# Performance work log

Hardware: AMD Instinct MI355X
Metric: run time of the kernel (lower is better)

The kernel has to match this reference:

```python
import jax, jax.numpy as jnp
import numpy as np
from jax import lax

SOS_TOKEN = 0
PAD_LEN = 30  # tokenizer.pad_len -> number of greedy decode steps


def _gru_cell(x, h, w_ih, w_hh, b_ih, b_hh):
    # PyTorch GRU cell math. x,h: [B,H]; w_*: [3H,H]; b_*: [3H]
    gi = x @ w_ih.T + b_ih
    gh = h @ w_hh.T + b_hh
    i_r, i_z, i_n = jnp.split(gi, 3, axis=-1)
    h_r, h_z, h_n = jnp.split(gh, 3, axis=-1)
    r = jax.nn.sigmoid(i_r + h_r)
    z = jax.nn.sigmoid(i_z + h_z)
    n = jnp.tanh(i_n + r * h_n)
    return (1.0 - z) * n + z * h


def _sm_encode(sm_hidden, conv_w, conv_b, enc_w, enc_b):
    # sm_hidden: [B, L, C] -> conv over time with C input channels
    x = jnp.transpose(sm_hidden, (0, 2, 1))  # [B, C, L]
    conv = lax.conv_general_dilated(
        x, conv_w, window_strides=(1,), padding='VALID',
        dimension_numbers=('NCH', 'OIH', 'NCH'))  # [B, O, L-k+1]
    conv = jax.nn.relu(conv + conv_b[None, :, None])
    pooled = jnp.max(conv, axis=-1)  # [B, O]
    return jax.nn.relu(pooled @ enc_w.T + enc_b)  # [B, H]


def reference(sm_hidden, embedding, w_ih, w_hh, b_ih, b_hh,
              w_out, b_out, conv_w, conv_b, enc_w, enc_b):
    B = sm_hidden.shape[0]
    h0 = _sm_encode(sm_hidden, conv_w, conv_b, enc_w, enc_b)  # [B, H]

    # The original re-runs the GRU over the whole (append-only) prefix each
    # iteration; since the GRU is deterministic this equals incremental
    # single-step updates, which we do here.
    def step(carry, _):
        h, tok = carry
        emb = embedding[tok]                      # [B, H]
        h_new = _gru_cell(emb, h, w_ih, w_hh, b_ih, b_hh)
        logits = h_new @ w_out.T + b_out          # [B, V]
        tok_new = jnp.argmax(logits, axis=-1)     # greedy topk(1)
        return (h_new, tok_new), (h_new, tok_new)

    tok0 = jnp.full((B,), SOS_TOKEN, dtype=jnp.int32)
    (h_last, _), (hiddens, toks) = lax.scan(step, (h0, tok0), None, length=PAD_LEN)

    decoder_output = jax.nn.log_softmax(h_last @ w_out.T + b_out, axis=1)  # [B, V]
    decoder_hidden = hiddens  # [PAD_LEN, B, H] == rnn_out of final _base_forward
    decoded_indices = jnp.concatenate([tok0[None, :], toks], axis=0)  # [PAD_LEN+1, B]
    return decoder_output, decoder_hidden, decoded_indices


def setup_inputs() -> dict:
    key = jax.random.key(0)
    ks = jax.random.split(key, 12)
    B, L, C = 512, 120, 128
    H, V, O, K = 1024, 512, 32, 10
    s = 1.0 / np.sqrt(H)
    return {
        'sm_hidden': jax.random.normal(ks[0], (B, L, C), jnp.float32),
        'embedding': jax.random.normal(ks[1], (V, H), jnp.float32),
        'w_ih': jax.random.uniform(ks[2], (3 * H, H), jnp.float32, -s, s),
        'w_hh': jax.random.uniform(ks[3], (3 * H, H), jnp.float32, -s, s),
        'b_ih': jax.random.uniform(ks[4], (3 * H,), jnp.float32, -s, s),
        'b_hh': jax.random.uniform(ks[5], (3 * H,), jnp.float32, -s, s),
        'w_out': jax.random.uniform(ks[6], (V, H), jnp.float32, -s, s),
        'b_out': jax.random.uniform(ks[7], (V,), jnp.float32, -s, s),
        'conv_w': jax.random.normal(ks[8], (O, C, K), jnp.float32) * 0.05,
        'conv_b': jax.random.normal(ks[9], (O,), jnp.float32) * 0.05,
        'enc_w': jax.random.uniform(ks[10], (H, O), jnp.float32, -s, s),
        'enc_b': jax.random.uniform(ks[11], (H,), jnp.float32, -s, s),
    }
```

## Files before the change

kernel.cpp:

```cpp
#include <hip/hip_runtime.h>
#include <hip/hip_bf16.h>
#include <math.h>

#define Bsz 512
#define Hd 1024
#define Vd 512
#define Cc 128
#define Ll 120
#define Kk 10
#define Oo 32
#define NSTEP 30

typedef __attribute__((ext_vector_type(8))) short bf16x8;
typedef __attribute__((ext_vector_type(4))) float f32x4;
typedef unsigned short ushort;
typedef unsigned long long u64;

static __device__ __forceinline__ float sigm(float x) { return 1.f / (1.f + expf(-x)); }
static __device__ __forceinline__ ushort f2bf(float x) {
    __hip_bfloat16 h = __float2bfloat16(x);
    return *(ushort*)&h;
}
static __device__ __forceinline__ float bf2f(ushort u) {
    __hip_bfloat16 h; *(ushort*)&h = u;
    return __bfloat162float(h);
}
static __device__ __forceinline__ unsigned monofy(float f) {
    unsigned u = __float_as_uint(f);
    return (u & 0x80000000u) ? ~u : (u | 0x80000000u);
}

__global__ void k_pack(const float* __restrict__ W, ushort* __restrict__ hi,
                       ushort* __restrict__ lo, int total) {
    int idx = blockIdx.x * 256 + threadIdx.x;
    if (idx >= total) return;
    int jj = idx & 7, l = (idx >> 3) & 63, c = (idx >> 9) & 31, nf = idx >> 14;
    int n = nf * 16 + (l & 15);
    int k = c * 32 + ((l >> 4) << 3) + jj;
    float v = W[(size_t)n * 1024 + k];
    ushort h = f2bf(v);
    hi[idx] = h;
    lo[idx] = f2bf(v - bf2f(h));
}

__global__ void k_packconv(const float* __restrict__ cw, ushort* __restrict__ hi,
                           ushort* __restrict__ lo) {
    int idx = blockIdx.x * 256 + threadIdx.x;
    if (idx >= 2 * 40 * 64 * 8) return;
    int jj = idx & 7, l = (idx >> 3) & 63, ch = (idx >> 9) % 40, nf = idx / (40 * 512);
    int o = nf * 16 + (l & 15);
    int k = ch * 32 + ((l >> 4) << 3) + jj;
    int kc = k >> 7, c = k & 127;
    float v = cw[(o * Cc + c) * Kk + kc];
    ushort h = f2bf(v);
    hi[idx] = h;
    lo[idx] = f2bf(v - bf2f(h));
}

__global__ __launch_bounds__(256) void k_convmfma(const float* __restrict__ sm,
                                                  const ushort* __restrict__ wH,
                                                  const ushort* __restrict__ wL,
                                                  const float* __restrict__ cb,
                                                  const float* __restrict__ ew,
                                                  const float* __restrict__ eb,
                                                  float* __restrict__ h0,
                                                  ushort* __restrict__ ApHi,
                                                  ushort* __restrict__ ApLo) {
    __shared__ ushort hiS[137 * 128];
    __shared__ ushort loS[137 * 128];
    __shared__ float sred[4][2][16];
    __shared__ float ps[Oo];
    int b = blockIdx.x, tid = threadIdx.x, wid = tid >> 6, l = tid & 63;

    const float* smb = sm + (size_t)b * (Ll * Cc);
    for (int i = tid; i < 1920; i += 256) {
        int row = i >> 4, col0 = (i & 15) * 8;
        float4 fa = *(const float4*)(smb + row * Cc + col0);
        float4 fb = *(const float4*)(smb + row * Cc + col0 + 4);
        float vv[8] = {fa.x, fa.y, fa.z, fa.w, fb.x, fb.y, fb.z, fb.w};
        ushort h8[8], l8[8];
#pragma unroll
        for (int q = 0; q < 8; ++q) {
            ushort h = f2bf(vv[q]);
            h8[q] = h;
            l8[q] = f2bf(vv[q] - bf2f(h));
        }
        int o = ((row << 8) + (col0 << 1)) ^ ((row & 7) << 4);
        *(bf16x8*)((char*)hiS + o) = *(bf16x8*)h8;
        *(bf16x8*)((char*)loS + o) = *(bf16x8*)l8;
    }
    __syncthreads();

    f32x4 acc[2][2];
#pragma unroll
    for (int i = 0; i < 2; ++i)
#pragma unroll
        for (int j = 0; j < 2; ++j) acc[i][j] = (f32x4)0.f;

    bf16x8 aH0[2], aL0[2], bH0[2], bL0[2];
    bf16x8 aH1[2], aL1[2], bH1[2], bL1[2];

#define CLD(AH, AL, BH, BL, ch)                                                        \
    {                                                                                  \
        _Pragma("unroll") for (int tf2 = 0; tf2 < 2; ++tf2) {                          \
            int row = (wid * 2 + tf2) * 16 + (l & 15) + ((ch) >> 2);                   \
            int o = ((row << 8) + ((((ch) & 3) * 32 + ((l >> 4) << 3)) << 1))          \
                    ^ ((row & 7) << 4);                                                \
            AH[tf2] = *(const bf16x8*)((const char*)hiS + o);                          \
            AL[tf2] = *(const bf16x8*)((const char*)loS + o);                          \
        }                                                                              \
        _Pragma("unroll") for (int nf = 0; nf < 2; ++nf) {                             \
            int boff = ((nf * 40 + (ch)) * 64 + l) * 8;                                \
            BH[nf] = *(const bf16x8*)(wH + boff);                                      \
            BL[nf] = *(const bf16x8*)(wL + boff);                                      \
        }                                                                              \
    }
#define CST(AH, AL, BH, BL)                                                            \
    {                                                                                  \
        _Pragma("unroll") for (int tf2 = 0; tf2 < 2; ++tf2)                            \
            _Pragma("unroll") for (int nf = 0; nf < 2; ++nf) {                         \
                acc[tf2][nf] = __builtin_amdgcn_mfma_f32_16x16x32_bf16(                \
                    AH[tf2], BH[nf], acc[tf2][nf], 0, 0, 0);                           \
                acc[tf2][nf] = __builtin_amdgcn_mfma_f32_16x16x32_bf16(                \
                    AH[tf2], BL[nf], acc[tf2][nf], 0, 0, 0);                           \
                acc[tf2][nf] = __builtin_amdgcn_mfma_f32_16x16x32_bf16(                \
                    AL[tf2], BH[nf], acc[tf2][nf], 0, 0, 0);                           \
            }                                                                          \
    }

    CLD(aH0, aL0, bH0, bL0, 0)
#pragma unroll
    for (int ch = 0; ch < 40; ch += 2) {
        CLD(aH1, aL1, bH1, bL1, ch + 1)
        CST(aH0, aL0, bH0, bL0)
        if (ch + 2 < 40) CLD(aH0, aL0, bH0, bL0, ch + 2)
        CST(aH1, aL1, bH1, bL1)
    }
#undef CLD
#undef CST

    float mx[2] = {-1e38f, -1e38f};
#pragma unroll
    for (int tf2 = 0; tf2 < 2; ++tf2) {
        int tb = (wid * 2 + tf2) * 16 + ((l >> 4) << 2);
#pragma unroll
        for (int q = 0; q < 4; ++q) {
            if (tb + q <= 110) {
                mx[0] = fmaxf(mx[0], acc[tf2][0][q]);
                mx[1] = fmaxf(mx[1], acc[tf2][1][q]);
            }
        }
    }
#pragma unroll
    for (int s = 16; s < 64; s <<= 1) {
        mx[0] = fmaxf(mx[0], __shfl_xor(mx[0], s));
        mx[1] = fmaxf(mx[1], __shfl_xor(mx[1], s));
    }
    if (l < 16) {
        sred[wid][0][l] = mx[0];
        sred[wid][1][l] = mx[1];
    }
    __syncthreads();
    if (tid < Oo) {
        float m = sred[0][tid >> 4][tid & 15];
#pragma unroll
        for (int w = 1; w < 4; ++w) m = fmaxf(m, sred[w][tid >> 4][tid & 15]);
        ps[tid] = fmaxf(m + cb[tid], 0.f);
    }
    __syncthreads();
    for (int j = tid; j < Hd; j += 256) {
        float a = eb[j];
        const float4* e4 = (const float4*)(ew + (size_t)j * Oo);
#pragma unroll
        for (int c4 = 0; c4 < 8; ++c4) {
            float4 w = e4[c4];
            a += ps[c4 * 4 + 0] * w.x + ps[c4 * 4 + 1] * w.y +
                 ps[c4 * 4 + 2] * w.z + ps[c4 * 4 + 3] * w.w;
        }
        a = fmaxf(a, 0.f);
        h0[(size_t)b * Hd + j] = a;
        ushort hb = f2bf(a);
        ushort lb = f2bf(a - bf2f(hb));
        int c = j >> 5, sub = (j >> 3) & 3, jj = j & 7, amf = b >> 4;
        int lane_r = (b & 15) + (sub << 4);
        int flat = ((amf * 32 + c) * 64 + lane_r) * 8 + jj;
        ApHi[flat] = hb;
        ApLo[flat] = lb;
    }
}

template <int EPI>
__global__ __launch_bounds__(512, 2) void k_rnn(const ushort* __restrict__ Ah,
                                                const ushort* __restrict__ Al,
                                                const ushort* __restrict__ Bh,
                                                const ushort* __restrict__ Bl,
                                                const float* __restrict__ bias,
                                                float* __restrict__ outF,
                                                const float* __restrict__ gi_all,
                                                const u64* __restrict__ pkRd,
                                                u64* __restrict__ pkWr,
                                                float* __restrict__ outIdxRow,
                                                const float* __restrict__ hOld,
                                                ushort* __restrict__ ApHi,
                                                ushort* __restrict__ ApLo) {
    __shared__ ushort Bs[2][48][512];
    int id = blockIdx.x;
    int xcd = id & 7, r = id >> 3;
    int jt = xcd * 4 + (r & 3);
    int mt = r >> 2;
    int tid = threadIdx.x, wid = tid >> 6, l = tid & 63;
    int wm = wid >> 1, wj = wid & 1;
    int mf = mt * 4 + wm;
    int jf = jt * 2 + wj;
    int jcol = jf * 16 + (l & 15);

    float giR[4][3], hR[4];
    int bR[4], tkR[4];
    if constexpr (EPI == 1) {
#pragma unroll
        for (int q = 0; q < 4; ++q) {
            bR[q] = mf * 16 + ((l >> 4) << 2) + q;
            u64 pk = pkRd[bR[q]];
            tkR[q] = 511 - (int)(unsigned)(pk & 0xFFFFFFFFu);
            const float* gi = gi_all + (size_t)tkR[q] * 3072;
            giR[q][0] = gi[jcol];
            giR[q][1] = gi[1024 + jcol];
            giR[q][2] = gi[2048 + jcol];
            hR[q] = hOld[(size_t)bR[q] * 1024 + jcol];
        }
        if (jt == 0 && wj == 0 && (l & 15) == 0) {
#pragma unroll
            for (int q = 0; q < 4; ++q) {
                pkWr[bR[q]] = 0ULL;
                if (outIdxRow) outIdxRow[bR[q]] = (float)tkR[q];
            }
        }
    }

    f32x4 acc[3];
#pragma unroll
    for (int g = 0; g < 3; ++g) acc[g] = (f32x4)0.f;

    bf16x8 stg[6], aH0[4], aL0[4], aH1[4], aL1[4];

#define STG_LD(it)                                                                     \
    {                                                                                  \
        _Pragma("unroll") for (int k = 0; k < 6; ++k) {                                \
            int u = wid + 8 * k;                                                       \
            int hl = u & 1, wjb = (u >> 1) & 1, g = (u >> 2) % 3, cu = u / 12;         \
            const ushort* sp = hl ? Bl : Bh;                                           \
            stg[k] = *(const bf16x8*)(sp +                                             \
                (size_t)(((g * 64 + jt * 2 + wjb) * 32 + (it) * 4 + cu) * 64 + l) * 8);\
        }                                                                              \
    }
#define STG_WR(buf)                                                                    \
    {                                                                                  \
        _Pragma("unroll") for (int k = 0; k < 6; ++k)                                  \
            *(bf16x8*)&Bs[buf][wid + 8 * k][l * 8] = stg[k];                           \
    }
#define A_LD(DH, DL, it)                                                               \
    {                                                                                  \
        _Pragma("unroll") for (int cc = 0; cc < 4; ++cc) {                             \
            DH[cc] = *(const bf16x8*)(Ah + (size_t)((mf * 32 + (it) * 4 + cc) * 64 + l) * 8); \
            DL[cc] = *(const bf16x8*)(Al + (size_t)((mf * 32 + (it) * 4 + cc) * 64 + l) * 8); \
        }                                                                              \
    }
#define CMP(buf, AH, AL)                                                               \
    {                                                                                  \
        _Pragma("unroll") for (int cc = 0; cc < 4; ++cc)                               \
            _Pragma("unroll") for (int g = 0; g < 3; ++g) {                            \
                bf16x8 bhh = *(const bf16x8*)&Bs[buf][cc * 12 + g * 4 + wj * 2 + 0][l * 8]; \
                bf16x8 bll = *(const bf16x8*)&Bs[buf][cc * 12 + g * 4 + wj * 2 + 1][l * 8]; \
                acc[g] = __builtin_amdgcn_mfma_f32_16x16x32_bf16(AH[cc], bhh, acc[g], 0, 0, 0); \
                acc[g] = __builtin_amdgcn_mfma_f32_16x16x32_bf16(AH[cc], bll, acc[g], 0, 0, 0); \
                acc[g] = __builtin_amdgcn_mfma_f32_16x16x32_bf16(AL[cc], bhh, acc[g], 0, 0, 0); \
            }                                                                          \
    }

    STG_LD(0)
    STG_WR(0)
    STG_LD(1)
    A_LD(aH0, aL0, 0)
    __syncthreads();
#pragma unroll
    for (int it = 0; it < 8; ++it) {
        int buf = it & 1;
        if (it < 7) STG_WR(buf ^ 1)
        if (it < 6) STG_LD(it + 2)
        if (it & 1) {
            if (it < 7) A_LD(aH0, aL0, it + 1)
            CMP(buf, aH1, aL1)
        } else {
            if (it < 7) A_LD(aH1, aL1, it + 1)
            CMP(buf, aH0, aL0)
        }
        __syncthreads();
    }
#undef STG_LD
#undef STG_WR
#undef A_LD
#undef CMP

    if constexpr (EPI == 0) {
#pragma unroll
        for (int q = 0; q < 4; ++q) {
            int b = mf * 16 + ((l >> 4) << 2) + q;
#pragma unroll
            for (int g = 0; g < 3; ++g)
                outF[(size_t)b * 3072 + g * 1024 + jcol] =
                    acc[g][q] + bias[g * 1024 + jcol];
        }
    } else {
        float bj0 = bias[jcol], bj1 = bias[1024 + jcol], bj2 = bias[2048 + jcol];
        int c = jcol >> 5, sub = (jcol >> 3) & 3, jj = jcol & 7;
#pragma unroll
        for (int q = 0; q < 4; ++q) {
            int b = bR[q];
            float rr = sigm(giR[q][0] + acc[0][q] + bj0);
            float zz = sigm(giR[q][1] + acc[1][q] + bj1);
            float nn = tanhf(giR[q][2] + rr * (acc[2][q] + bj2));
            float hv = (1.f - zz) * nn + zz * hR[q];
            outF[(size_t)b * 1024 + jcol] = hv;
            ushort hb = f2bf(hv);
            ushort lb = f2bf(hv - bf2f(hb));
            int lane_r = (b & 15) + (sub << 4);
            int flat = (((b >> 4) * 32 + c) * 64 + lane_r) * 8 + jj;
            ApHi[flat] = hb;
            ApLo[flat] = lb;
        }
    }
}

__global__ __launch_bounds__(256) void k_lgt(const ushort* __restrict__ Ah,
                                             const ushort* __restrict__ Al,
                                             const ushort* __restrict__ Bh,
                                             const ushort* __restrict__ Bl,
                                             const float* __restrict__ bias,
                                             float* __restrict__ outF,
                                             u64* __restrict__ pkOut) {
    int p = blockIdx.x * 4 + (threadIdx.x >> 6);
    int l = threadIdx.x & 63;
    int mf = p >> 5, vf = p & 31;
    size_t ab = (size_t)(mf * 32) * 512 + l * 8;
    size_t bb = (size_t)(vf * 32) * 512 + l * 8;
    f32x4 acc = (f32x4)0.f;
    bf16x8 a0h, a0l, b0h, b0l, a1h, a1l, b1h, b1l;

#define LD1(AH, AL, BH, BL, c)                                                         \
    {                                                                                  \
        AH = *(const bf16x8*)(Ah + ab + (size_t)(c) * 512);                            \
        AL = *(const bf16x8*)(Al + ab + (size_t)(c) * 512);                            \
        BH = *(const bf16x8*)(Bh + bb + (size_t)(c) * 512);                            \
        BL = *(const bf16x8*)(Bl + bb + (size_t)(c) * 512);                            \
    }
#define ST1(AH, AL, BH, BL)                                                            \
    {                                                                                  \
        acc = __builtin_amdgcn_mfma_f32_16x16x32_bf16(AH, BH, acc, 0, 0, 0);           \
        acc = __builtin_amdgcn_mfma_f32_16x16x32_bf16(AH, BL, acc, 0, 0, 0);           \
        acc = __builtin_amdgcn_mfma_f32_16x16x32_bf16(AL, BH, acc, 0, 0, 0);           \
    }

    LD1(a0h, a0l, b0h, b0l, 0)
#pragma unroll
    for (int c = 0; c < 32; c += 2) {
        LD1(a1h, a1l, b1h, b1l, c + 1)
        ST1(a0h, a0l, b0h, b0l)
        if (c + 2 < 32) LD1(a0h, a0l, b0h, b0l, c + 2)
        ST1(a1h, a1l, b1h, b1l)
    }
#undef LD1
#undef ST1

    int v = vf * 16 + (l & 15);
    float bv = bias[v];
    float lg[4];
    unsigned vmq[4];
#pragma unroll
    for (int q = 0; q < 4; ++q) {
        int b = mf * 16 + ((l >> 4) << 2) + q;
        lg[q] = acc[q] + bv;
        outF[(size_t)b * Vd + v] = lg[q];
        vmq[q] = 511u - (unsigned)v;
    }
#pragma unroll
    for (int off = 1; off < 16; off <<= 1) {
#pragma unroll
        for (int q = 0; q < 4; ++q) {
            float og = __shfl_xor(lg[q], off);
            unsigned ov = __shfl_xor(vmq[q], off);
            if (og > lg[q] || (og == lg[q] && ov > vmq[q])) { lg[q] = og; vmq[q] = ov; }
        }
    }
    if ((l & 15) == 0) {
#pragma unroll
        for (int q = 0; q < 4; ++q) {
            int b = mf * 16 + ((l >> 4) << 2) + q;
            u64 pk = ((u64)monofy(lg[q]) << 32) | (u64)vmq[q];
            atomicMax(&pkOut[b], pk);
        }
    }
}

__global__ __launch_bounds__(64) void k_fin(const float* __restrict__ logits,
                                            const u64* __restrict__ pk,
                                            float* __restrict__ out_lsm,
                                            float* __restrict__ outIdxRow) {
    int b = blockIdx.x, l = threadIdx.x;
    const float* row = logits + (size_t)b * Vd;
    float bv = -3.4e38f;
#pragma unroll
    for (int s = 0; s < 8; ++s) bv = fmaxf(bv, row[s * 64 + l]);
#pragma unroll
    for (int off = 1; off < 64; off <<= 1) bv = fmaxf(bv, __shfl_xor(bv, off));
    float sum = 0.f;
#pragma unroll
    for (int s = 0; s < 8; ++s) sum += expf(row[s * 64 + l] - bv);
#pragma unroll
    for (int off = 1; off < 64; off <<= 1) sum += __shfl_xor(sum, off);
    float lse = logf(sum) + bv;
#pragma unroll
    for (int s = 0; s < 8; ++s) {
        int v = s * 64 + l;
        out_lsm[(size_t)b * Vd + v] = row[v] - lse;
    }
    if (l == 0)
        outIdxRow[b] = (float)(511 - (int)(unsigned)(pk[b] & 0xFFFFFFFFu));
}

__global__ void k_init(u64* __restrict__ P0, float* __restrict__ out_idx0) {
    int i = blockIdx.x * 64 + threadIdx.x;
    if (i < Bsz) {
        P0[i] = (1ULL << 32) | 511ULL;
        out_idx0[i] = 0.f;
    }
}

extern "C" void kernel_launch(void* const* d_in, const int* in_sizes, int n_in,
                              void* d_out, int out_size, void* d_ws, size_t ws_size,
                              hipStream_t stream) {
    const float* sm    = (const float*)d_in[0];
    const float* emb   = (const float*)d_in[1];
    const float* w_ih  = (const float*)d_in[2];
    const float* w_hh  = (const float*)d_in[3];
    const float* b_ih  = (const float*)d_in[4];
    const float* b_hh  = (const float*)d_in[5];
    const float* w_out = (const float*)d_in[6];
    const float* b_out = (const float*)d_in[7];
    const float* cw    = (const float*)d_in[8];
    const float* cb    = (const float*)d_in[9];
    const float* ew    = (const float*)d_in[10];
    const float* eb    = (const float*)d_in[11];

    float* out0 = (float*)d_out;
    float* out1 = out0 + (size_t)Bsz * Vd;
    float* out2 = out1 + (size_t)NSTEP * Bsz * Hd;

    char* wsp = (char*)d_ws;
    float*  f_gi  = (float*)wsp;  wsp += sizeof(float) * Bsz * 3072;
    float*  f_h0  = (float*)wsp;  wsp += sizeof(float) * Bsz * Hd;
    float*  f_log = (float*)wsp;  wsp += sizeof(float) * Bsz * Vd;
    u64*    Ppk0  = (u64*)wsp;    wsp += sizeof(u64) * Bsz;
    u64*    Ppk1  = (u64*)wsp;    wsp += sizeof(u64) * Bsz;
    ushort* ApHi0 = (ushort*)wsp; wsp += sizeof(ushort) * Bsz * Hd;
    ushort* ApLo0 = (ushort*)wsp; wsp += sizeof(ushort) * Bsz * Hd;
    ushort* ApHi1 = (ushort*)wsp; wsp += sizeof(ushort) * Bsz * Hd;
    ushort* ApLo1 = (ushort*)wsp; wsp += sizeof(ushort) * Bsz * Hd;
    ushort* embH  = (ushort*)wsp; wsp += sizeof(ushort) * Vd * Hd;
    ushort* embL  = (ushort*)wsp; wsp += sizeof(ushort) * Vd * Hd;
    ushort* wihH  = (ushort*)wsp; wsp += sizeof(ushort) * 3072 * Hd;
    ushort* wihL  = (ushort*)wsp; wsp += sizeof(ushort) * 3072 * Hd;
    ushort* whhH  = (ushort*)wsp; wsp += sizeof(ushort) * 3072 * Hd;
    ushort* whhL  = (ushort*)wsp; wsp += sizeof(ushort) * 3072 * Hd;
    ushort* woutH = (ushort*)wsp; wsp += sizeof(ushort) * Vd * Hd;
    ushort* woutL = (ushort*)wsp; wsp += sizeof(ushort) * Vd * Hd;
    ushort* cwBH  = (ushort*)wsp; wsp += sizeof(ushort) * 2 * 40 * 64 * 8;
    ushort* cwBL  = (ushort*)wsp; wsp += sizeof(ushort) * 2 * 40 * 64 * 8;

    k_packconv<<<160, 256, 0, stream>>>(cw, cwBH, cwBL);
    k_pack<<<(3072 * 1024) / 256, 256, 0, stream>>>(w_ih, wihH, wihL, 3072 * 1024);
    k_pack<<<(3072 * 1024) / 256, 256, 0, stream>>>(w_hh, whhH, whhL, 3072 * 1024);
    k_pack<<<(512 * 1024) / 256, 256, 0, stream>>>(w_out, woutH, woutL, 512 * 1024);
    k_pack<<<(512 * 1024) / 256, 256, 0, stream>>>(emb, embH, embL, 512 * 1024);
    k_convmfma<<<Bsz, 256, 0, stream>>>(sm, cwBH, cwBL, cb, ew, eb,
                                        f_h0, ApHi0, ApLo0);
    k_rnn<0><<<256, 512, 0, stream>>>(embH, embL, wihH, wihL, b_ih, f_gi,
                                      nullptr, nullptr, nullptr, nullptr, nullptr,
                                      nullptr, nullptr);
    k_init<<<8, 64, 0, stream>>>(Ppk0, out2);

    ushort* aH[2] = {ApHi0, ApHi1};
    ushort* aL[2] = {ApLo0, ApLo1};
    u64* P[2] = {Ppk0, Ppk1};
    for (int t = 0; t < NSTEP; ++t) {
        int cur = t & 1, nxt = cur ^ 1;
        const float* hOld = (t == 0) ? f_h0 : (out1 + (size_t)(t - 1) * Bsz * Hd);
        k_rnn<1><<<256, 512, 0, stream>>>(
            aH[cur], aL[cur], whhH, whhL, b_hh, out1 + (size_t)t * Bsz * Hd,
            f_gi, P[t & 1], P[(t + 1) & 1],
            (t >= 1) ? (out2 + (size_t)t * Bsz) : nullptr,
            hOld, aH[nxt], aL[nxt]);
        k_lgt<<<256, 256, 0, stream>>>(aH[nxt], aL[nxt], woutH, woutL, b_out,
                                       f_log, P[(t + 1) & 1]);
    }
    k_fin<<<Bsz, 64, 0, stream>>>(f_log, P[NSTEP & 1], out0,
                                  out2 + (size_t)NSTEP * Bsz);
}
```

Before: 835.9 us.

## Stage logits weights in LDS, widen conv blocks, skip redundant logit stores

The logits kernel now stages w_out tiles in double-buffered shared memory. Blocks are mapped so that four warps share one vocab tile, and each block id is distributed across XCDs. The conv kernel moves to 512 threads with one M-tile per warp. The full logits are written only on the last step, and __syncthreads is replaced by a barrier that waits only on LDS counters. Together these aim to cut redundant global loads and stores in the per-step decode loop, at the cost of extra barriers and LDS traffic.

```diff
diff --git a/kernel.cpp b/kernel.cpp
--- a/kernel.cpp
+++ b/kernel.cpp
@@ -15,6 +15,8 @@
 typedef __attribute__((ext_vector_type(4))) float f32x4;
 typedef unsigned short ushort;
 typedef unsigned long long u64;
+
+#define BARLDS() asm volatile("s_waitcnt lgkmcnt(0)\n\ts_barrier" ::: "memory")
 
 static __device__ __forceinline__ float sigm(float x) { return 1.f / (1.f + expf(-x)); }
 static __device__ __forceinline__ ushort f2bf(float x) {
@@ -57,7 +59,7 @@
     lo[idx] = f2bf(v - bf2f(h));
 }
 
-__global__ __launch_bounds__(256) void k_convmfma(const float* __restrict__ sm,
+__global__ __launch_bounds__(512) void k_convmfma(const float* __restrict__ sm,
                                                   const ushort* __restrict__ wH,
                                                   const ushort* __restrict__ wL,
                                                   const float* __restrict__ cb,
@@ -68,12 +70,12 @@
                                                   ushort* __restrict__ ApLo) {
     __shared__ ushort hiS[137 * 128];
     __shared__ ushort loS[137 * 128];
-    __shared__ float sred[4][2][16];
+    __shared__ float sred[8][2][16];
     __shared__ float ps[Oo];
     int b = blockIdx.x, tid = threadIdx.x, wid = tid >> 6, l = tid & 63;
 
     const float* smb = sm + (size_t)b * (Ll * Cc);
-    for (int i = tid; i < 1920; i += 256) {
+    for (int i = tid; i < 1920; i += 512) {
         int row = i >> 4, col0 = (i & 15) * 8;
         float4 fa = *(const float4*)(smb + row * Cc + col0);
         float4 fb = *(const float4*)(smb + row * Cc + col0 + 4);
@@ -91,24 +93,20 @@
     }
     __syncthreads();
 
-    f32x4 acc[2][2];
-#pragma unroll
-    for (int i = 0; i < 2; ++i)
-#pragma unroll
-        for (int j = 0; j < 2; ++j) acc[i][j] = (f32x4)0.f;
-
-    bf16x8 aH0[2], aL0[2], bH0[2], bL0[2];
-    bf16x8 aH1[2], aL1[2], bH1[2], bL1[2];
+    f32x4 acc[2];
+#pragma unroll
+    for (int j = 0; j < 2; ++j) acc[j] = (f32x4)0.f;
+
+    bf16x8 aH0, aL0, bH0[2], bL0[2];
+    bf16x8 aH1, aL1, bH1[2], bL1[2];
 
 #define CLD(AH, AL, BH, BL, ch)                                                        \
     {                                                                                  \
-        _Pragma("unroll") for (int tf2 = 0; tf2 < 2; ++tf2) {                          \
-            int row = (wid * 2 + tf2) * 16 + (l & 15) + ((ch) >> 2);                   \
-            int o = ((row << 8) + ((((ch) & 3) * 32 + ((l >> 4) << 3)) << 1))          \
-                    ^ ((row & 7) << 4);                                                \
-            AH[tf2] = *(const bf16x8*)((const char*)hiS + o);                          \
-            AL[tf2] = *(const bf16x8*)((const char*)loS + o);                          \
-        }                                                                              \
+        int row = wid * 16 + (l & 15) + ((ch) >> 2);                                   \
+        int o = ((row << 8) + ((((ch) & 3) * 32 + ((l >> 4) << 3)) << 1))              \
+                ^ ((row & 7) << 4);                                                    \
+        AH = *(const bf16x8*)((const char*)hiS + o);                                   \
+        AL = *(const bf16x8*)((const char*)loS + o);                                   \
         _Pragma("unroll") for (int nf = 0; nf < 2; ++nf) {                             \
             int boff = ((nf * 40 + (ch)) * 64 + l) * 8;                                \
             BH[nf] = *(const bf16x8*)(wH + boff);                                      \
@@ -117,15 +115,11 @@
     }
 #define CST(AH, AL, BH, BL)                                                            \
     {                                                                                  \
-        _Pragma("unroll") for (int tf2 = 0; tf2 < 2; ++tf2)                            \
-            _Pragma("unroll") for (int nf = 0; nf < 2; ++nf) {                         \
-                acc[tf2][nf] = __builtin_amdgcn_mfma_f32_16x16x32_bf16(                \
-                    AH[tf2], BH[nf], acc[tf2][nf], 0, 0, 0);                           \
-                acc[tf2][nf] = __builtin_amdgcn_mfma_f32_16x16x32_bf16(                \
-                    AH[tf2], BL[nf], acc[tf2][nf], 0, 0, 0);                           \
-                acc[tf2][nf] = __builtin_amdgcn_mfma_f32_16x16x32_bf16(                \
-                    AL[tf2], BH[nf], acc[tf2][nf], 0, 0, 0);                           \
-            }                                                                          \
+        _Pragma("unroll") for (int nf = 0; nf < 2; ++nf) {                             \
+            acc[nf] = __builtin_amdgcn_mfma_f32_16x16x32_bf16(AH, BH[nf], acc[nf], 0, 0, 0); \
+            acc[nf] = __builtin_amdgcn_mfma_f32_16x16x32_bf16(AH, BL[nf], acc[nf], 0, 0, 0); \
+            acc[nf] = __builtin_amdgcn_mfma_f32_16x16x32_bf16(AL, BH[nf], acc[nf], 0, 0, 0); \
+        }                                                                              \
     }
 
     CLD(aH0, aL0, bH0, bL0, 0)
@@ -140,14 +134,13 @@
 #undef CST
 
     float mx[2] = {-1e38f, -1e38f};
-#pragma unroll
-    for (int tf2 = 0; tf2 < 2; ++tf2) {
-        int tb = (wid * 2 + tf2) * 16 + ((l >> 4) << 2);
+    {
+        int tb = wid * 16 + ((l >> 4) << 2);
 #pragma unroll
         for (int q = 0; q < 4; ++q) {
             if (tb + q <= 110) {
-                mx[0] = fmaxf(mx[0], acc[tf2][0][q]);
-                mx[1] = fmaxf(mx[1], acc[tf2][1][q]);
+                mx[0] = fmaxf(mx[0], acc[0][q]);
+                mx[1] = fmaxf(mx[1], acc[1][q]);
             }
         }
     }
@@ -164,11 +157,11 @@
     if (tid < Oo) {
         float m = sred[0][tid >> 4][tid & 15];
 #pragma unroll
-        for (int w = 1; w < 4; ++w) m = fmaxf(m, sred[w][tid >> 4][tid & 15]);
+        for (int w = 1; w < 8; ++w) m = fmaxf(m, sred[w][tid >> 4][tid & 15]);
         ps[tid] = fmaxf(m + cb[tid], 0.f);
     }
     __syncthreads();
-    for (int j = tid; j < Hd; j += 256) {
+    for (int j = tid; j < Hd; j += 512) {
         float a = eb[j];
         const float4* e4 = (const float4*)(ew + (size_t)j * Oo);
 #pragma unroll
@@ -281,7 +274,7 @@
     STG_WR(0)
     STG_LD(1)
     A_LD(aH0, aL0, 0)
-    __syncthreads();
+    BARLDS();
 #pragma unroll
     for (int it = 0; it < 8; ++it) {
         int buf = it & 1;
@@ -294,7 +287,7 @@
             if (it < 7) A_LD(aH1, aL1, it + 1)
             CMP(buf, aH0, aL0)
         }
-        __syncthreads();
+        BARLDS();
     }
 #undef STG_LD
 #undef STG_WR
@@ -338,38 +331,79 @@
                                              const float* __restrict__ bias,
                                              float* __restrict__ outF,
                                              u64* __restrict__ pkOut) {
-    int p = blockIdx.x * 4 + (threadIdx.x >> 6);
-    int l = threadIdx.x & 63;
-    int mf = p >> 5, vf = p & 31;
-    size_t ab = (size_t)(mf * 32) * 512 + l * 8;
-    size_t bb = (size_t)(vf * 32) * 512 + l * 8;
+    __shared__ ushort Bs[2][8][512];
+    int id = blockIdx.x;
+    int xcd = id & 7, r = id >> 3;
+    int vf = xcd * 4 + (r & 3);
+    int mg = r >> 2;
+    int tid = threadIdx.x, w = tid >> 6, l = tid & 63;
+    int mf = mg * 4 + w;
+
     f32x4 acc = (f32x4)0.f;
-    bf16x8 a0h, a0l, b0h, b0l, a1h, a1l, b1h, b1l;
-
-#define LD1(AH, AL, BH, BL, c)                                                         \
-    {                                                                                  \
-        AH = *(const bf16x8*)(Ah + ab + (size_t)(c) * 512);                            \
-        AL = *(const bf16x8*)(Al + ab + (size_t)(c) * 512);                            \
-        BH = *(const bf16x8*)(Bh + bb + (size_t)(c) * 512);                            \
-        BL = *(const bf16x8*)(Bl + bb + (size_t)(c) * 512);                            \
-    }
-#define ST1(AH, AL, BH, BL)                                                            \
-    {                                                                                  \
-        acc = __builtin_amdgcn_mfma_f32_16x16x32_bf16(AH, BH, acc, 0, 0, 0);           \
-        acc = __builtin_amdgcn_mfma_f32_16x16x32_bf16(AH, BL, acc, 0, 0, 0);           \
-        acc = __builtin_amdgcn_mfma_f32_16x16x32_bf16(AL, BH, acc, 0, 0, 0);           \
-    }
-
-    LD1(a0h, a0l, b0h, b0l, 0)
-#pragma unroll
-    for (int c = 0; c < 32; c += 2) {
-        LD1(a1h, a1l, b1h, b1l, c + 1)
-        ST1(a0h, a0l, b0h, b0l)
-        if (c + 2 < 32) LD1(a0h, a0l, b0h, b0l, c + 2)
-        ST1(a1h, a1l, b1h, b1l)
-    }
-#undef LD1
-#undef ST1
+    bf16x8 stg[2];
+    bf16x8 a0h[4], a0l[4], a1h[4], a1l[4];
+
+#define LSTG_LD(it)                                                                    \
+    {                                                                                  \
+        _Pragma("unroll") for (int k = 0; k < 2; ++k) {                                \
+            int s = tid + 256 * k;                                                     \
+            int il = s & 63, u = s >> 6;                                               \
+            int hl = u & 1, cu = u >> 1;                                               \
+            const ushort* sp = hl ? Bl : Bh;                                           \
+            stg[k] = *(const bf16x8*)(sp +                                             \
+                (size_t)((vf * 32 + (it) * 4 + cu) * 64 + il) * 8);                    \
+        }                                                                              \
+    }
+#define LSTG_WR(buf)                                                                   \
+    {                                                                                  \
+        _Pragma("unroll") for (int k = 0; k < 2; ++k) {                                \
+            int s = tid + 256 * k;                                                     \
+            int il = s & 63, u = s >> 6;                                               \
+            *(bf16x8*)&Bs[buf][u][il * 8] = stg[k];                                    \
+        }                                                                              \
+    }
+#define LA_LD(DH, DL, it)                                                              \
+    {                                                                                  \
+        _Pragma("unroll") for (int cu = 0; cu < 4; ++cu) {                             \
+            size_t aoff = (size_t)((mf * 32 + (it) * 4 + cu) * 64 + l) * 8;            \
+            DH[cu] = *(const bf16x8*)(Ah + aoff);                                      \
+            DL[cu] = *(const bf16x8*)(Al + aoff);                                      \
+        }                                                                              \
+    }
+#define LCMP(buf, AH, AL)                                                              \
+    {                                                                                  \
+        _Pragma("unroll") for (int cu = 0; cu < 4; ++cu) {                             \
+            bf16x8 bh = *(const bf16x8*)&Bs[buf][cu * 2 + 0][l * 8];                   \
+            bf16x8 bl = *(const bf16x8*)&Bs[buf][cu * 2 + 1][l * 8];                   \
+            acc = __builtin_amdgcn_mfma_f32_16x16x32_bf16(AH[cu], bh, acc, 0, 0, 0);   \
+            acc = __builtin_amdgcn_mfma_f32_16x16x32_bf16(AH[cu], bl, acc, 0, 0, 0);   \
+            acc = __builtin_amdgcn_mfma_f32_16x16x32_bf16(AL[cu], bh, acc, 0, 0, 0);   \
+        }                                                                              \
+    }
+
+    LSTG_LD(0)
+    LSTG_WR(0)
+    LSTG_LD(1)
+    LA_LD(a0h, a0l, 0)
+    BARLDS();
+#pragma unroll
+    for (int it = 0; it < 8; ++it) {
+        int buf = it & 1;
+        if (it < 7) LSTG_WR(buf ^ 1)
+        if (it < 6) LSTG_LD(it + 2)
+        if (it & 1) {
+            if (it < 7) LA_LD(a0h, a0l, it + 1)
+            LCMP(buf, a1h, a1l)
+        } else {
+            if (it < 7) LA_LD(a1h, a1l, it + 1)
+            LCMP(buf, a0h, a0l)
+        }
+        BARLDS();
+    }
+#undef LSTG_LD
+#undef LSTG_WR
+#undef LA_LD
+#undef LCMP
 
     int v = vf * 16 + (l & 15);
     float bv = bias[v];
@@ -379,7 +413,7 @@
     for (int q = 0; q < 4; ++q) {
         int b = mf * 16 + ((l >> 4) << 2) + q;
         lg[q] = acc[q] + bv;
-        outF[(size_t)b * Vd + v] = lg[q];
+        if (outF) outF[(size_t)b * Vd + v] = lg[q];
         vmq[q] = 511u - (unsigned)v;
     }
 #pragma unroll
@@ -481,7 +515,7 @@
     k_pack<<<(3072 * 1024) / 256, 256, 0, stream>>>(w_hh, whhH, whhL, 3072 * 1024);
     k_pack<<<(512 * 1024) / 256, 256, 0, stream>>>(w_out, woutH, woutL, 512 * 1024);
     k_pack<<<(512 * 1024) / 256, 256, 0, stream>>>(emb, embH, embL, 512 * 1024);
-    k_convmfma<<<Bsz, 256, 0, stream>>>(sm, cwBH, cwBL, cb, ew, eb,
+    k_convmfma<<<Bsz, 512, 0, stream>>>(sm, cwBH, cwBL, cb, ew, eb,
                                         f_h0, ApHi0, ApLo0);
     k_rnn<0><<<256, 512, 0, stream>>>(embH, embL, wihH, wihL, b_ih, f_gi,
                                       nullptr, nullptr, nullptr, nullptr, nullptr,
@@ -500,7 +534,8 @@
             (t >= 1) ? (out2 + (size_t)t * Bsz) : nullptr,
             hOld, aH[nxt], aL[nxt]);
         k_lgt<<<256, 256, 0, stream>>>(aH[nxt], aL[nxt], woutH, woutL, b_out,
-                                       f_log, P[(t + 1) & 1]);
+                                       (t == NSTEP - 1) ? f_log : nullptr,
+                                       P[(t + 1) & 1]);
     }
     k_fin<<<Bsz, 64, 0, stream>>>(f_log, P[NSTEP & 1], out0,
                                   out2 + (size_t)NSTEP * Bsz);
```

Result: faster. 779.8 us (-6.7%).
